# Kernel optimization log

Measured on AMD Instinct MI355X. Metric: run time of the kernel, lower is better.

Reference implementation:

```python
import jax, jax.numpy as jnp
import numpy as np

M_PARAM = 8          # M from __init__
NUM_INTERESTS = 32   # K, num_extracted_interests (max)


def setup_inputs() -> dict:
    key = jax.random.key(0)
    ks = jax.random.split(key, 6)
    bs, L, N, d, ic, K = 512, 100, 64, 256, 256, NUM_INTERESTS
    history = jax.random.normal(ks[0], (bs, L, d), dtype=jnp.float32)
    history_mask = jnp.ones((bs, L), dtype=bool)  # unused by the original forward, kept for signature fidelity
    candidates = jax.random.normal(ks[1], (bs, N, d), dtype=jnp.float32)
    num_extracted_interests = jnp.maximum(
        jax.random.randint(ks[2], (bs,), 0, K, dtype=jnp.int32), 1)
    unique_category_counts = jax.random.randint(ks[3], (bs,), 1, 19, dtype=jnp.int32)
    W = jax.random.normal(ks[4], (ic, d), dtype=jnp.float32) / np.sqrt(d)   # Linear(news_dim->interest_dim), no bias
    context_codes = jax.random.normal(ks[5], (K, ic), dtype=jnp.float32) / np.sqrt(ic)
    return {
        "history_news_representations": history,
        "history_mask": history_mask,
        "candidate_news_representations": candidates,
        "num_extracted_interests": num_extracted_interests,
        "unique_category_counts": unique_category_counts,
        "W": W,
        "context_codes": context_codes,
    }


def _user_encoder(history, candidates, num_interests, cat_counts, W, context_codes):
    bs, L, d = history.shape
    K = context_codes.shape[0]
    # ---- PolyAttention ----
    proj = jnp.tanh(jnp.einsum('bld,cd->blc', history, W))           # [bs, L, ic]
    scores = jnp.einsum('blc,kc->bkl', proj, context_codes)          # [bs, K, L]
    code_mask = jnp.arange(K)[None, :] < num_interests[:, None]      # [bs, K]
    scores = jnp.where(code_mask[:, :, None], scores, jnp.float32(-1e9))
    attn = jax.nn.softmax(scores, axis=2)                            # over history length L
    attn = jnp.nan_to_num(attn, nan=0.0, posinf=0.0, neginf=0.0)
    interests = jnp.einsum('bkl,bld->bkd', attn, history)            # [bs, K, d]
    # ---- InterestCandidateAttention, vectorized over all N candidates ----
    w = jnp.einsum('bkd,bnd->bnk', interests, candidates)            # [bs, N, K]
    dynK = jnp.clip(
        jnp.ceil(jnp.log2(M_PARAM * cat_counts.astype(jnp.float32))).astype(jnp.int32),
        1, K)                                                        # [bs]
    # variable-K top-k mask via descending ranks (values a.s. distinct)
    order = jnp.argsort(-w, axis=-1)
    ranks = jnp.argsort(order, axis=-1)                              # rank 0 = largest
    topk_mask = (ranks < dynK[:, None, None]).astype(w.dtype)        # [bs, N, K]
    masked = w * topk_mask
    user = jnp.einsum('bnk,bkd->bnd', masked, interests)             # [bs, N, d]
    return user


def reference(history_news_representations, history_mask, candidate_news_representations,
              num_extracted_interests, unique_category_counts, W, context_codes):
    return _user_encoder(history_news_representations, candidate_news_representations,
                         num_extracted_interests, unique_category_counts, W, context_codes)
```

## Files before the change

kernel.cpp:

```cpp
#include <hip/hip_runtime.h>
#include <hip/hip_bf16.h>

typedef __bf16 bf16_t;
typedef __bf16 bf16x8 __attribute__((ext_vector_type(8)));
typedef float  f32x4  __attribute__((ext_vector_type(4)));

#define BS 512
#define LH 100
#define NC 64
#define DD 256
#define IC 256
#define KK 32

#define OFF_WPL 6553600
#define OFF_CPL (6553600 + 3 * 131072)

__device__ __forceinline__ void split3(float v, bf16_t& h, bf16_t& l, bf16_t& l2) {
    h = (bf16_t)v;  float r1 = v - (float)h;
    l = (bf16_t)r1; float r2 = r1 - (float)l;
    l2 = (bf16_t)r2;
}

__device__ __forceinline__ void split3x8(const float* v, bf16x8& h, bf16x8& l, bf16x8& l2) {
#pragma unroll
    for (int j = 0; j < 8; j++) {
        bf16_t a, b, c;
        split3(v[j], a, b, c);
        h[j] = a; l[j] = b; l2[j] = c;
    }
}

__device__ __forceinline__ void mfma6(const bf16x8& ah, const bf16x8& al, const bf16x8& al2,
                                      const bf16x8& bh, const bf16x8& bl, const bf16x8& bl2,
                                      f32x4& accM, f32x4& accC) {
    accM = __builtin_amdgcn_mfma_f32_16x16x32_bf16(ah,  bh,  accM, 0, 0, 0);
    accC = __builtin_amdgcn_mfma_f32_16x16x32_bf16(ah,  bl,  accC, 0, 0, 0);
    accC = __builtin_amdgcn_mfma_f32_16x16x32_bf16(al,  bh,  accC, 0, 0, 0);
    accC = __builtin_amdgcn_mfma_f32_16x16x32_bf16(ah,  bl2, accC, 0, 0, 0);
    accC = __builtin_amdgcn_mfma_f32_16x16x32_bf16(al,  bl,  accC, 0, 0, 0);
    accC = __builtin_amdgcn_mfma_f32_16x16x32_bf16(al2, bh,  accC, 0, 0, 0);
}

__device__ __forceinline__ void mfma6s(const bf16x8& ah, const bf16x8& al, const bf16x8& al2,
                                       const bf16x8& bh, const bf16x8& bl, const bf16x8& bl2,
                                       f32x4& accM, f32x4& accC0, f32x4& accC1) {
    accM  = __builtin_amdgcn_mfma_f32_16x16x32_bf16(ah,  bh,  accM,  0, 0, 0);
    accC0 = __builtin_amdgcn_mfma_f32_16x16x32_bf16(ah,  bl,  accC0, 0, 0, 0);
    accC1 = __builtin_amdgcn_mfma_f32_16x16x32_bf16(al,  bh,  accC1, 0, 0, 0);
    accC0 = __builtin_amdgcn_mfma_f32_16x16x32_bf16(ah,  bl2, accC0, 0, 0, 0);
    accC1 = __builtin_amdgcn_mfma_f32_16x16x32_bf16(al,  bl,  accC1, 0, 0, 0);
    accC0 = __builtin_amdgcn_mfma_f32_16x16x32_bf16(al2, bh,  accC0, 0, 0, 0);
}

__device__ __forceinline__ float fast_tanh_f32(float xf) {
    const double t  = fabs((double)xf) * 2.0;
    const double nf = rint(t * 1.4426950408889634);
    double r = fma(nf, -6.93147180369123816490e-01, t);
    r = fma(nf, -1.90821492927058770002e-10, r);
    const double r2 = r * r;
    double p =        2.08767569878680989792e-09;
    p = fma(p, r,     2.50521083854417187751e-08);
    p = fma(p, r,     2.75573192239858906526e-07);
    p = fma(p, r,     2.75573192239858925110e-06);
    p = fma(p, r,     2.48015873015873015873e-05);
    p = fma(p, r,     1.98412698412698412526e-04);
    p = fma(p, r,     1.38888888888888894069e-03);
    p = fma(p, r,     8.33333333333333321769e-03);
    p = fma(p, r,     4.16666666666666643537e-02);
    p = fma(p, r,     1.66666666666666657415e-01);
    p = fma(p, r,     5.00000000000000000000e-01);
    const double q   = fma(r2, p, r);
    const double s   = ldexp(1.0, (int)nf);
    const double em1 = fma(s, q, s - 1.0);
    double ti = em1 / (em1 + 2.0);
    if (t > 20.0) ti = 1.0;
    return copysignf((float)ti, xf);
}

__device__ __forceinline__ double fast_exp_f64(double x) {
    const double nf = rint(x * 1.4426950408889634);
    double r = fma(nf, -6.93147180369123816490e-01, x);
    r = fma(nf, -1.90821492927058770002e-10, r);
    const double r2 = r * r;
    double p =        2.08767569878680989792e-09;
    p = fma(p, r,     2.50521083854417187751e-08);
    p = fma(p, r,     2.75573192239858906526e-07);
    p = fma(p, r,     2.75573192239858925110e-06);
    p = fma(p, r,     2.48015873015873015873e-05);
    p = fma(p, r,     1.98412698412698412526e-04);
    p = fma(p, r,     1.38888888888888894069e-03);
    p = fma(p, r,     8.33333333333333321769e-03);
    p = fma(p, r,     4.16666666666666643537e-02);
    p = fma(p, r,     1.66666666666666657415e-01);
    p = fma(p, r,     5.00000000000000000000e-01);
    const double q = fma(r2, p, r);
    const double s = ldexp(1.0, (int)nf);
    return fma(s, q, s);
}

__global__ __launch_bounds__(256) void kp_split(const float* __restrict__ W,
                                                const float* __restrict__ C,
                                                bf16_t* __restrict__ Wh, bf16_t* __restrict__ Wl,
                                                bf16_t* __restrict__ Wl2,
                                                bf16_t* __restrict__ Ch, bf16_t* __restrict__ Cl,
                                                bf16_t* __restrict__ Cl2) {
    int idx = blockIdx.x * 256 + threadIdx.x;
    if (idx < 65536) {
        bf16_t h, l, l2;
        split3(W[idx], h, l, l2);
        Wh[idx] = h; Wl[idx] = l; Wl2[idx] = l2;
    } else {
        int i = idx - 65536;
        if (i < 8192) {
            bf16_t h, l, l2;
            split3(C[i], h, l, l2);
            Ch[i] = h; Cl[i] = l; Cl2[i] = l2;
        }
    }
}

#define WCH 24576
__global__ __launch_bounds__(448) void k12_proj_scores(const float* __restrict__ H,
                                                       const bf16_t* __restrict__ Wh,
                                                       const bf16_t* __restrict__ Wl,
                                                       const bf16_t* __restrict__ Wl2,
                                                       const bf16_t* __restrict__ Ch,
                                                       const bf16_t* __restrict__ Cl,
                                                       const bf16_t* __restrict__ Cl2,
                                                       float* __restrict__ S) {
    __shared__ __align__(16) char wbuf[2][WCH];
    __shared__ float pl[7][16 * 34];

    const int tid = threadIdx.x;
    const int wave = tid >> 6;
    const int lane = tid & 63;
    const int r = lane & 15, q = lane >> 4;
    const int b = blockIdx.x;
    const int lrow0 = wave * 16;

    const bf16_t* it_base[4];
    int it_src[4], it_dst[4];
#pragma unroll
    for (int it = 0; it < 4; it++) {
        const int g = tid + it * 448;
        const int p = (g >> 9) & 3, rem = g & 511, row = rem >> 5, grp = rem & 31;
        it_base[it] = (p == 0) ? Wh : (p == 1) ? Wl : Wl2;
        it_src[it] = row * DD + grp * 8;
        it_dst[it] = (p * 16 + row) * 512 + ((grp * 16) ^ ((row & 7) << 4));
    }
    const bool has4 = (tid < 192);

    bf16x8 Ah[8], Al[8], Al2[8];
    {
        long grow = (long)b * LH + lrow0 + r;
        const long maxrow = (long)BS * LH - 1;
        if (grow > maxrow) grow = maxrow;
        const float* arow = H + (size_t)grow * DD + q * 8;
#pragma unroll
        for (int ks = 0; ks < 8; ks++) {
            const float* ap = arow + ks * 32;
            float4 u = *(const float4*)ap;
            float4 v = *(const float4*)(ap + 4);
            float av[8] = {u.x, u.y, u.z, u.w, v.x, v.y, v.z, v.w};
            split3x8(av, Ah[ks], Al[ks], Al2[ks]);
        }
    }

    const f32x4 zero = {0.f, 0.f, 0.f, 0.f};
    f32x4 saccM[2], saccC[2];
    saccM[0] = zero; saccM[1] = zero; saccC[0] = zero; saccC[1] = zero;

    float* myp = pl[wave];
    const int swz = (r & 7) << 4;

    {
        bf16x8 p0 = *(const bf16x8*)(it_base[0] + it_src[0]);
        bf16x8 p1 = *(const bf16x8*)(it_base[1] + it_src[1]);
        bf16x8 p2 = *(const bf16x8*)(it_base[2] + it_src[2]);
        bf16x8 p3;
        if (has4) p3 = *(const bf16x8*)(it_base[3] + it_src[3]);
        *(bf16x8*)(wbuf[0] + it_dst[0]) = p0;
        *(bf16x8*)(wbuf[0] + it_dst[1]) = p1;
        *(bf16x8*)(wbuf[0] + it_dst[2]) = p2;
        if (has4) *(bf16x8*)(wbuf[0] + it_dst[3]) = p3;
    }
    __syncthreads();

    for (int c16 = 0; c16 < 16; c16++) {
        const char* cur = wbuf[c16 & 1];
        char* nxt = wbuf[(c16 & 1) ^ 1];
        const bool pfv = (c16 < 15);

        bf16x8 p0, p1, p2, p3;
        if (pfv) {
            const int co = (c16 + 1) * 16 * DD;
            p0 = *(const bf16x8*)(it_base[0] + co + it_src[0]);
            p1 = *(const bf16x8*)(it_base[1] + co + it_src[1]);
            p2 = *(const bf16x8*)(it_base[2] + co + it_src[2]);
            if (has4) p3 = *(const bf16x8*)(it_base[3] + co + it_src[3]);
        }

        f32x4 aM = zero, aC0 = zero, aC1 = zero;
#pragma unroll
        for (int ks = 0; ks < 8; ks++) {
            const int colb = (ks * 64 + q * 16) ^ swz;
            const char* rowp = cur + r * 512 + colb;
            bf16x8 bh  = *(const bf16x8*)(rowp);
            bf16x8 bl  = *(const bf16x8*)(rowp + 8192);
            bf16x8 bl2 = *(const bf16x8*)(rowp + 16384);
            mfma6s(Ah[ks], Al[ks], Al2[ks], bh, bl, bl2, aM, aC0, aC1);
        }

        const int colb2 = (c16 & 1) * 16;
#pragma unroll
        for (int i = 0; i < 4; i++) {
            float s1 = aM[i] + aC0[i] + aC1[i];
            myp[(q * 4 + i) * 34 + colb2 + r] = fast_tanh_f32(s1);
        }

        if (c16 & 1) {
            const int c0 = (c16 >> 1) * 32;
            const float* ps = myp + r * 34 + q * 8;
            float pv[8];
#pragma unroll
            for (int j = 0; j < 8; j++) pv[j] = ps[j];
            bf16x8 ph, plo, pl2;
            split3x8(pv, ph, plo, pl2);
#pragma unroll
            for (int ntS = 0; ntS < 2; ntS++) {
                const size_t base = (size_t)(ntS * 16 + r) * IC + c0 + q * 8;
                bf16x8 ch  = *(const bf16x8*)(Ch  + base);
                bf16x8 cl  = *(const bf16x8*)(Cl  + base);
                bf16x8 cl2 = *(const bf16x8*)(Cl2 + base);
                mfma6(ph, plo, pl2, ch, cl, cl2, saccM[ntS], saccC[ntS]);
            }
        }

        if (pfv) {
            *(bf16x8*)(nxt + it_dst[0]) = p0;
            *(bf16x8*)(nxt + it_dst[1]) = p1;
            *(bf16x8*)(nxt + it_dst[2]) = p2;
            if (has4) *(bf16x8*)(nxt + it_dst[3]) = p3;
        }
        __syncthreads();
    }

#pragma unroll
    for (int ntS = 0; ntS < 2; ntS++)
#pragma unroll
        for (int i = 0; i < 4; i++) {
            const int lrow = lrow0 + q * 4 + i;
            if (lrow < LH)
                S[((size_t)b * LH + lrow) * KK + ntS * 16 + r] = saccM[ntS][i] + saccC[ntS][i];
        }
}

__global__ __launch_bounds__(512) void k3456_fused(const float* __restrict__ Sg,
                                                   const int* __restrict__ ni,
                                                   const int* __restrict__ cc,
                                                   const float* __restrict__ H,
                                                   const float* __restrict__ cand,
                                                   float* __restrict__ out) {
    __shared__ __align__(16) char smem[47616];
    float*  attn_l = (float*)smem;
    float*  ls     = (float*)(smem + 12800);
    double* red    = (double*)(smem + 25600);
    float*  ht     = (float*)(smem + 12800);
    float*  I_l    = (float*)(smem + 12800);
    float*  shw    = (float*)smem;

    const int b = blockIdx.x;
    const int tid = threadIdx.x;
    const int wave = tid >> 6;
    const int lane = tid & 63;
    const int r = lane & 15, q = lane >> 4;
    const f32x4 zero = {0.f, 0.f, 0.f, 0.f};

    {
        const float* Sb = Sg + (size_t)b * LH * KK;
        for (int i = tid; i < LH * KK; i += 512) ls[i] = Sb[i];
        __syncthreads();

        const int k = tid & 31;
        const int grp = tid >> 5;
        const bool act = (grp < 8);
        const int nib = ni[b];

        double vals[13];
        if (act) {
            double vmax = -1e300;
#pragma unroll
            for (int i = 0; i < 13; i++) {
                const int l = grp + 8 * i;
                double v = (l < LH) ? (double)ls[l * KK + k] : -1e300;
                vals[i] = v;
                vmax = fmax(vmax, v);
            }
            red[grp * 33 + k] = vmax;
        }
        __syncthreads();
        if (tid < 32) {
            double m = red[k];
            for (int j = 1; j < 8; j++) m = fmax(m, red[j * 33 + k]);
            red[k] = m;
        }
        __syncthreads();
        const double mx = red[k];
        __syncthreads();

        if (act) {
            double s = 0.0;
#pragma unroll
            for (int i = 0; i < 13; i++) {
                const int l = grp + 8 * i;
                if (l < LH) {
                    double e = fast_exp_f64(vals[i] - mx);
                    vals[i] = e;
                    s += e;
                }
            }
            red[grp * 33 + k] = s;
        }
        __syncthreads();
        if (tid < 32) {
            double t = 0.0;
            for (int j = 0; j < 8; j++) t += red[j * 33 + k];
            red[k] = t;
        }
        __syncthreads();
        const double inv = 1.0 / red[k];

        if (act) {
            float* ab = attn_l + k * LH;
            const bool masked = (k >= nib);
#pragma unroll
            for (int i = 0; i < 13; i++) {
                const int l = grp + 8 * i;
                if (l < LH) ab[l] = masked ? 0.01f : (float)(vals[i] * inv);
            }
        }
    }
    __syncthreads();

    {
        const float* Hb = H + (size_t)b * LH * DD;
        const int mtB = wave & 1;
        const int m0B = mtB * 16;

        f32x4 accM[4], accC[4];
#pragma unroll
        for (int jj = 0; jj < 4; jj++) { accM[jj] = zero; accC[jj] = zero; }

        for (int ks = 0; ks < 4; ks++) {
            const int l0c = ks * 32;
            __syncthreads();
            for (int u = tid; u < 32 * 64; u += 512) {
                const int l = u >> 6, dg = u & 63;
                float4 v = {0.f, 0.f, 0.f, 0.f};
                if (l0c + l < LH) v = *(const float4*)(Hb + (size_t)(l0c + l) * DD + dg * 4);
                ht[(dg * 4 + 0) * 34 + l] = v.x;
                ht[(dg * 4 + 1) * 34 + l] = v.y;
                ht[(dg * 4 + 2) * 34 + l] = v.z;
                ht[(dg * 4 + 3) * 34 + l] = v.w;
            }
            __syncthreads();

            float av[8];
#pragma unroll
            for (int j = 0; j < 8; j++) {
                const int l = l0c + q * 8 + j;
                av[j] = (l < LH) ? attn_l[(m0B + r) * LH + l] : 0.f;
            }
            bf16x8 ah, al, al2;
            split3x8(av, ah, al, al2);

#pragma unroll
            for (int jj = 0; jj < 4; jj++) {
                const int job = wave + jj * 8;
                const int nt = job >> 1;
                const int n0 = nt * 16;
                float bv[8];
                const float* hp = ht + (n0 + r) * 34 + q * 8;
#pragma unroll
                for (int j = 0; j < 8; j++) bv[j] = hp[j];
                bf16x8 bh, bl, bl2;
                split3x8(bv, bh, bl, bl2);
                mfma6(ah, al, al2, bh, bl, bl2, accM[jj], accC[jj]);
            }
        }
        __syncthreads();

#pragma unroll
        for (int jj = 0; jj < 4; jj++) {
            const int job = wave + jj * 8;
            const int nt = job >> 1;
            const int n0 = nt * 16;
#pragma unroll
            for (int i = 0; i < 4; i++)
                I_l[(m0B + q * 4 + i) * 260 + n0 + r] = accM[jj][i] + accC[jj][i];
        }
    }
    __syncthreads();

    {
        const float* Cb = cand + (size_t)b * NC * DD;
        const int job = wave;
        const int mt = job >> 1, nt = job & 1;
        const int m0 = mt * 16, n0 = nt * 16;
        f32x4 accM = zero, accC = zero;
#pragma unroll
        for (int ks = 0; ks < 8; ks++) {
            const float* ap = Cb + (size_t)(m0 + r) * DD + ks * 32 + q * 8;
            const float* bp = I_l + (n0 + r) * 260 + ks * 32 + q * 8;
            float4 u1 = *(const float4*)ap;      float4 u2 = *(const float4*)(ap + 4);
            float4 v1 = *(const float4*)bp;      float4 v2 = *(const float4*)(bp + 4);
            float av[8] = {u1.x,u1.y,u1.z,u1.w,u2.x,u2.y,u2.z,u2.w};
            float bv[8] = {v1.x,v1.y,v1.z,v1.w,v2.x,v2.y,v2.z,v2.w};
            bf16x8 ah, al, al2, bh, bl, bl2;
            split3x8(av, ah, al, al2);
            split3x8(bv, bh, bl, bl2);
            mfma6(ah, al, al2, bh, bl, bl2, accM, accC);
        }
#pragma unroll
        for (int i = 0; i < 4; i++) shw[(m0 + q * 4 + i) * 33 + n0 + r] = accM[i] + accC[i];

        __syncthreads();

        {
            const int n = tid & 63;
            const int kg = tid >> 6;
            int c8 = 8 * cc[b];
            int dynK = 32 - __clz(c8 - 1);
            dynK = min(max(dynK, 1), KK);
            float v[KK];
#pragma unroll
            for (int j = 0; j < KK; j++) v[j] = shw[n * 33 + j];
            float keep[4];
#pragma unroll
            for (int j = 0; j < 4; j++) {
                const int kk2 = kg + 8 * j;
                int rank = 0;
#pragma unroll
                for (int jj = 0; jj < KK; jj++)
                    rank += (v[jj] > v[kk2]) || (v[jj] == v[kk2] && jj < kk2);
                keep[j] = (rank < dynK) ? v[kk2] : 0.f;
            }
            __syncthreads();
#pragma unroll
            for (int j = 0; j < 4; j++)
                shw[n * 33 + kg + 8 * j] = keep[j];
        }
    }
    __syncthreads();

    {
        const int d = tid & 255;
        const int nh = tid >> 8;
        float icol[KK];
#pragma unroll
        for (int k = 0; k < KK; k++) icol[k] = I_l[k * 260 + d];

        const int nend = nh * 32 + 32;
        for (int n = nh * 32; n < nend; n++) {
            const float* wr = shw + n * 33;
            float acc = 0.f;
#pragma unroll
            for (int k = 0; k < KK; k++) acc += wr[k] * icol[k];
            out[((size_t)b * NC + n) * DD + d] = acc;
        }
    }
}

extern "C" void kernel_launch(void* const* d_in, const int* in_sizes, int n_in,
                              void* d_out, int out_size, void* d_ws, size_t ws_size,
                              hipStream_t stream) {
    const float* hist = (const float*)d_in[0];
    const float* cand = (const float*)d_in[2];
    const int* ni = (const int*)d_in[3];
    const int* cc = (const int*)d_in[4];
    const float* W = (const float*)d_in[5];
    const float* C = (const float*)d_in[6];
    float* out = (float*)d_out;

    char* w8 = (char*)d_ws;
    float*  S   = (float*)(w8 + 0);
    bf16_t* Wh  = (bf16_t*)(w8 + OFF_WPL);
    bf16_t* Wl  = (bf16_t*)(w8 + OFF_WPL + 131072);
    bf16_t* Wl2 = (bf16_t*)(w8 + OFF_WPL + 262144);
    bf16_t* Ch  = (bf16_t*)(w8 + OFF_CPL);
    bf16_t* Cl  = (bf16_t*)(w8 + OFF_CPL + 16384);
    bf16_t* Cl2 = (bf16_t*)(w8 + OFF_CPL + 32768);

    kp_split<<<288, 256, 0, stream>>>(W, C, Wh, Wl, Wl2, Ch, Cl, Cl2);
    k12_proj_scores<<<BS, 448, 0, stream>>>(hist, Wh, Wl, Wl2, Ch, Cl, Cl2, S);
    k3456_fused<<<BS, 512, 0, stream>>>(S, ni, cc, hist, cand, out);
}
```

Measured before the change: 232.0 us.

## Use a dedicated producer wave for W tile staging in proj-scores kernel

```diff
diff --git a/kernel.cpp b/kernel.cpp
--- a/kernel.cpp
+++ b/kernel.cpp
@@ -120,7 +120,7 @@
 }
 
 #define WCH 24576
-__global__ __launch_bounds__(448) void k12_proj_scores(const float* __restrict__ H,
+__global__ __launch_bounds__(512) void k12_proj_scores(const float* __restrict__ H,
                                                        const bf16_t* __restrict__ Wh,
                                                        const bf16_t* __restrict__ Wl,
                                                        const bf16_t* __restrict__ Wl2,
@@ -136,22 +136,25 @@
     const int lane = tid & 63;
     const int r = lane & 15, q = lane >> 4;
     const int b = blockIdx.x;
+    const bool producer = (wave == 7);
     const int lrow0 = wave * 16;
 
-    const bf16_t* it_base[4];
-    int it_src[4], it_dst[4];
-#pragma unroll
-    for (int it = 0; it < 4; it++) {
-        const int g = tid + it * 448;
-        const int p = (g >> 9) & 3, rem = g & 511, row = rem >> 5, grp = rem & 31;
-        it_base[it] = (p == 0) ? Wh : (p == 1) ? Wl : Wl2;
-        it_src[it] = row * DD + grp * 8;
-        it_dst[it] = (p * 16 + row) * 512 + ((grp * 16) ^ ((row & 7) << 4));
-    }
-    const bool has4 = (tid < 192);
+    const f32x4 zero = {0.f, 0.f, 0.f, 0.f};
+    f32x4 saccM[2], saccC[2];
+    saccM[0] = zero; saccM[1] = zero; saccC[0] = zero; saccC[1] = zero;
 
     bf16x8 Ah[8], Al[8], Al2[8];
-    {
+
+    if (producer) {
+#pragma unroll 4
+        for (int it = 0; it < 24; it++) {
+            const int g = lane + it * 64;
+            const int p = g >> 9, rem = g & 511, row = rem >> 5, grp = rem & 31;
+            const bf16_t* src = (p == 0) ? Wh : (p == 1) ? Wl : Wl2;
+            bf16x8 v = *(const bf16x8*)(src + row * DD + grp * 8);
+            *(bf16x8*)(wbuf[0] + (p * 16 + row) * 512 + ((grp * 16) ^ ((row & 7) << 4))) = v;
+        }
+    } else {
         long grow = (long)b * LH + lrow0 + r;
         const long maxrow = (long)BS * LH - 1;
         if (grow > maxrow) grow = maxrow;
@@ -165,94 +168,77 @@
             split3x8(av, Ah[ks], Al[ks], Al2[ks]);
         }
     }
-
-    const f32x4 zero = {0.f, 0.f, 0.f, 0.f};
-    f32x4 saccM[2], saccC[2];
-    saccM[0] = zero; saccM[1] = zero; saccC[0] = zero; saccC[1] = zero;
-
-    float* myp = pl[wave];
+    __syncthreads();
+
+    float* myp = pl[wave & 7];
     const int swz = (r & 7) << 4;
-
-    {
-        bf16x8 p0 = *(const bf16x8*)(it_base[0] + it_src[0]);
-        bf16x8 p1 = *(const bf16x8*)(it_base[1] + it_src[1]);
-        bf16x8 p2 = *(const bf16x8*)(it_base[2] + it_src[2]);
-        bf16x8 p3;
-        if (has4) p3 = *(const bf16x8*)(it_base[3] + it_src[3]);
-        *(bf16x8*)(wbuf[0] + it_dst[0]) = p0;
-        *(bf16x8*)(wbuf[0] + it_dst[1]) = p1;
-        *(bf16x8*)(wbuf[0] + it_dst[2]) = p2;
-        if (has4) *(bf16x8*)(wbuf[0] + it_dst[3]) = p3;
-    }
-    __syncthreads();
 
     for (int c16 = 0; c16 < 16; c16++) {
         const char* cur = wbuf[c16 & 1];
         char* nxt = wbuf[(c16 & 1) ^ 1];
-        const bool pfv = (c16 < 15);
-
-        bf16x8 p0, p1, p2, p3;
-        if (pfv) {
-            const int co = (c16 + 1) * 16 * DD;
-            p0 = *(const bf16x8*)(it_base[0] + co + it_src[0]);
-            p1 = *(const bf16x8*)(it_base[1] + co + it_src[1]);
-            p2 = *(const bf16x8*)(it_base[2] + co + it_src[2]);
-            if (has4) p3 = *(const bf16x8*)(it_base[3] + co + it_src[3]);
-        }
-
-        f32x4 aM = zero, aC0 = zero, aC1 = zero;
-#pragma unroll
-        for (int ks = 0; ks < 8; ks++) {
-            const int colb = (ks * 64 + q * 16) ^ swz;
-            const char* rowp = cur + r * 512 + colb;
-            bf16x8 bh  = *(const bf16x8*)(rowp);
-            bf16x8 bl  = *(const bf16x8*)(rowp + 8192);
-            bf16x8 bl2 = *(const bf16x8*)(rowp + 16384);
-            mfma6s(Ah[ks], Al[ks], Al2[ks], bh, bl, bl2, aM, aC0, aC1);
-        }
-
-        const int colb2 = (c16 & 1) * 16;
-#pragma unroll
-        for (int i = 0; i < 4; i++) {
-            float s1 = aM[i] + aC0[i] + aC1[i];
-            myp[(q * 4 + i) * 34 + colb2 + r] = fast_tanh_f32(s1);
-        }
-
-        if (c16 & 1) {
-            const int c0 = (c16 >> 1) * 32;
-            const float* ps = myp + r * 34 + q * 8;
-            float pv[8];
-#pragma unroll
-            for (int j = 0; j < 8; j++) pv[j] = ps[j];
-            bf16x8 ph, plo, pl2;
-            split3x8(pv, ph, plo, pl2);
-#pragma unroll
-            for (int ntS = 0; ntS < 2; ntS++) {
-                const size_t base = (size_t)(ntS * 16 + r) * IC + c0 + q * 8;
-                bf16x8 ch  = *(const bf16x8*)(Ch  + base);
-                bf16x8 cl  = *(const bf16x8*)(Cl  + base);
-                bf16x8 cl2 = *(const bf16x8*)(Cl2 + base);
-                mfma6(ph, plo, pl2, ch, cl, cl2, saccM[ntS], saccC[ntS]);
-            }
-        }
-
-        if (pfv) {
-            *(bf16x8*)(nxt + it_dst[0]) = p0;
-            *(bf16x8*)(nxt + it_dst[1]) = p1;
-            *(bf16x8*)(nxt + it_dst[2]) = p2;
-            if (has4) *(bf16x8*)(nxt + it_dst[3]) = p3;
-        }
-        __syncthreads();
-    }
-
-#pragma unroll
-    for (int ntS = 0; ntS < 2; ntS++)
-#pragma unroll
-        for (int i = 0; i < 4; i++) {
-            const int lrow = lrow0 + q * 4 + i;
-            if (lrow < LH)
-                S[((size_t)b * LH + lrow) * KK + ntS * 16 + r] = saccM[ntS][i] + saccC[ntS][i];
-        }
+
+        if (producer) {
+            if (c16 < 15) {
+                const int co = (c16 + 1) * 16 * DD;
+#pragma unroll 4
+                for (int it = 0; it < 24; it++) {
+                    const int g = lane + it * 64;
+                    const int p = g >> 9, rem = g & 511, row = rem >> 5, grp = rem & 31;
+                    const bf16_t* src = (p == 0) ? Wh : (p == 1) ? Wl : Wl2;
+                    bf16x8 v = *(const bf16x8*)(src + co + row * DD + grp * 8);
+                    *(bf16x8*)(nxt + (p * 16 + row) * 512 + ((grp * 16) ^ ((row & 7) << 4))) = v;
+                }
+            }
+        } else {
+            f32x4 aM = zero, aC0 = zero, aC1 = zero;
+#pragma unroll
+            for (int ks = 0; ks < 8; ks++) {
+                const int colb = (ks * 64 + q * 16) ^ swz;
+                const char* rowp = cur + r * 512 + colb;
+                bf16x8 bh  = *(const bf16x8*)(rowp);
+                bf16x8 bl  = *(const bf16x8*)(rowp + 8192);
+                bf16x8 bl2 = *(const bf16x8*)(rowp + 16384);
+                mfma6s(Ah[ks], Al[ks], Al2[ks], bh, bl, bl2, aM, aC0, aC1);
+            }
+
+            const int colb2 = (c16 & 1) * 16;
+#pragma unroll
+            for (int i = 0; i < 4; i++) {
+                float s1 = aM[i] + aC0[i] + aC1[i];
+                myp[(q * 4 + i) * 34 + colb2 + r] = fast_tanh_f32(s1);
+            }
+
+            if (c16 & 1) {
+                const int c0 = (c16 >> 1) * 32;
+                const float* ps = myp + r * 34 + q * 8;
+                float pv[8];
+#pragma unroll
+                for (int j = 0; j < 8; j++) pv[j] = ps[j];
+                bf16x8 ph, plo, pl2;
+                split3x8(pv, ph, plo, pl2);
+#pragma unroll
+                for (int ntS = 0; ntS < 2; ntS++) {
+                    const size_t base = (size_t)(ntS * 16 + r) * IC + c0 + q * 8;
+                    bf16x8 ch  = *(const bf16x8*)(Ch  + base);
+                    bf16x8 cl  = *(const bf16x8*)(Cl  + base);
+                    bf16x8 cl2 = *(const bf16x8*)(Cl2 + base);
+                    mfma6(ph, plo, pl2, ch, cl, cl2, saccM[ntS], saccC[ntS]);
+                }
+            }
+        }
+        __syncthreads();
+    }
+
+    if (!producer) {
+#pragma unroll
+        for (int ntS = 0; ntS < 2; ntS++)
+#pragma unroll
+            for (int i = 0; i < 4; i++) {
+                const int lrow = lrow0 + q * 4 + i;
+                if (lrow < LH)
+                    S[((size_t)b * LH + lrow) * KK + ntS * 16 + r] = saccM[ntS][i] + saccC[ntS][i];
+            }
+    }
 }
 
 __global__ __launch_bounds__(512) void k3456_fused(const float* __restrict__ Sg,
@@ -492,6 +478,6 @@
     bf16_t* Cl2 = (bf16_t*)(w8 + OFF_CPL + 32768);
 
     kp_split<<<288, 256, 0, stream>>>(W, C, Wh, Wl, Wl2, Ch, Cl, Cl2);
-    k12_proj_scores<<<BS, 448, 0, stream>>>(hist, Wh, Wl, Wl2, Ch, Cl, Cl2, S);
+    k12_proj_scores<<<BS, 512, 0, stream>>>(hist, Wh, Wl, Wl2, Ch, Cl, Cl2, S);
     k3456_fused<<<BS, 512, 0, stream>>>(S, ni, cc, hist, cand, out);
 }
```

Result: slower. 249.4 us (+7.5%).

## Process 32-column W chunks per iteration with single-buffered LDS staging

Applied to the files above, without the earlier changes.

```diff
diff --git a/kernel.cpp b/kernel.cpp
--- a/kernel.cpp
+++ b/kernel.cpp
@@ -119,7 +119,6 @@
     }
 }
 
-#define WCH 24576
 __global__ __launch_bounds__(448) void k12_proj_scores(const float* __restrict__ H,
                                                        const bf16_t* __restrict__ Wh,
                                                        const bf16_t* __restrict__ Wl,
@@ -128,7 +127,7 @@
                                                        const bf16_t* __restrict__ Cl,
                                                        const bf16_t* __restrict__ Cl2,
                                                        float* __restrict__ S) {
-    __shared__ __align__(16) char wbuf[2][WCH];
+    __shared__ __align__(16) char wbuf[49152];
     __shared__ float pl[7][16 * 34];
 
     const int tid = threadIdx.x;
@@ -138,17 +137,19 @@
     const int b = blockIdx.x;
     const int lrow0 = wave * 16;
 
-    const bf16_t* it_base[4];
-    int it_src[4], it_dst[4];
-#pragma unroll
-    for (int it = 0; it < 4; it++) {
+    const bf16_t* it_base[7];
+    int it_src[7], it_dst[7];
+#pragma unroll
+    for (int it = 0; it < 7; it++) {
         const int g = tid + it * 448;
-        const int p = (g >> 9) & 3, rem = g & 511, row = rem >> 5, grp = rem & 31;
+        const int p0 = g >> 10;
+        const int p = (p0 > 2) ? 2 : p0;
+        const int rem = g & 1023, row = rem >> 5, grp = rem & 31;
         it_base[it] = (p == 0) ? Wh : (p == 1) ? Wl : Wl2;
         it_src[it] = row * DD + grp * 8;
-        it_dst[it] = (p * 16 + row) * 512 + ((grp * 16) ^ ((row & 7) << 4));
-    }
-    const bool has4 = (tid < 192);
+        it_dst[it] = (p * 32 + row) * 512 + ((grp * 16) ^ ((row & 7) << 4));
+    }
+    const bool has7 = (tid < 384);
 
     bf16x8 Ah[8], Al[8], Al2[8];
     {
@@ -174,52 +175,55 @@
     const int swz = (r & 7) << 4;
 
     {
-        bf16x8 p0 = *(const bf16x8*)(it_base[0] + it_src[0]);
-        bf16x8 p1 = *(const bf16x8*)(it_base[1] + it_src[1]);
-        bf16x8 p2 = *(const bf16x8*)(it_base[2] + it_src[2]);
-        bf16x8 p3;
-        if (has4) p3 = *(const bf16x8*)(it_base[3] + it_src[3]);
-        *(bf16x8*)(wbuf[0] + it_dst[0]) = p0;
-        *(bf16x8*)(wbuf[0] + it_dst[1]) = p1;
-        *(bf16x8*)(wbuf[0] + it_dst[2]) = p2;
-        if (has4) *(bf16x8*)(wbuf[0] + it_dst[3]) = p3;
+#pragma unroll
+        for (int it = 0; it < 7; it++)
+            if (it < 6 || has7) {
+                bf16x8 v = *(const bf16x8*)(it_base[it] + it_src[it]);
+                *(bf16x8*)(wbuf + it_dst[it]) = v;
+            }
     }
     __syncthreads();
 
-    for (int c16 = 0; c16 < 16; c16++) {
-        const char* cur = wbuf[c16 & 1];
-        char* nxt = wbuf[(c16 & 1) ^ 1];
-        const bool pfv = (c16 < 15);
-
-        bf16x8 p0, p1, p2, p3;
-        if (pfv) {
-            const int co = (c16 + 1) * 16 * DD;
-            p0 = *(const bf16x8*)(it_base[0] + co + it_src[0]);
-            p1 = *(const bf16x8*)(it_base[1] + co + it_src[1]);
-            p2 = *(const bf16x8*)(it_base[2] + co + it_src[2]);
-            if (has4) p3 = *(const bf16x8*)(it_base[3] + co + it_src[3]);
-        }
-
-        f32x4 aM = zero, aC0 = zero, aC1 = zero;
+    for (int pr = 0; pr < 8; pr++) {
+        bf16x8 pf[7];
+        if (pr < 7) {
+            const int co = (pr + 1) * 8192;
+#pragma unroll
+            for (int it = 0; it < 7; it++)
+                if (it < 6 || has7)
+                    pf[it] = *(const bf16x8*)(it_base[it] + co + it_src[it]);
+        }
+
+        f32x4 aM0 = zero, aC00 = zero, aC01 = zero;
+        f32x4 aM1 = zero, aC10 = zero, aC11 = zero;
 #pragma unroll
         for (int ks = 0; ks < 8; ks++) {
             const int colb = (ks * 64 + q * 16) ^ swz;
-            const char* rowp = cur + r * 512 + colb;
-            bf16x8 bh  = *(const bf16x8*)(rowp);
-            bf16x8 bl  = *(const bf16x8*)(rowp + 8192);
-            bf16x8 bl2 = *(const bf16x8*)(rowp + 16384);
-            mfma6s(Ah[ks], Al[ks], Al2[ks], bh, bl, bl2, aM, aC0, aC1);
-        }
-
-        const int colb2 = (c16 & 1) * 16;
+            const char* b0 = wbuf + r * 512 + colb;
+            const char* b1 = wbuf + (16 + r) * 512 + colb;
+            bf16x8 bh0  = *(const bf16x8*)(b0);
+            bf16x8 bl0  = *(const bf16x8*)(b0 + 16384);
+            bf16x8 bl20 = *(const bf16x8*)(b0 + 32768);
+            bf16x8 bh1  = *(const bf16x8*)(b1);
+            bf16x8 bl1  = *(const bf16x8*)(b1 + 16384);
+            bf16x8 bl21 = *(const bf16x8*)(b1 + 32768);
+            mfma6s(Ah[ks], Al[ks], Al2[ks], bh0, bl0, bl20, aM0, aC00, aC01);
+            mfma6s(Ah[ks], Al[ks], Al2[ks], bh1, bl1, bl21, aM1, aC10, aC11);
+        }
+
 #pragma unroll
         for (int i = 0; i < 4; i++) {
-            float s1 = aM[i] + aC0[i] + aC1[i];
-            myp[(q * 4 + i) * 34 + colb2 + r] = fast_tanh_f32(s1);
-        }
-
-        if (c16 & 1) {
-            const int c0 = (c16 >> 1) * 32;
+            float s0 = aM0[i] + aC00[i] + aC01[i];
+            myp[(q * 4 + i) * 34 + r] = fast_tanh_f32(s0);
+        }
+#pragma unroll
+        for (int i = 0; i < 4; i++) {
+            float s1 = aM1[i] + aC10[i] + aC11[i];
+            myp[(q * 4 + i) * 34 + 16 + r] = fast_tanh_f32(s1);
+        }
+
+        {
+            const int c0 = pr * 32;
             const float* ps = myp + r * 34 + q * 8;
             float pv[8];
 #pragma unroll
@@ -236,11 +240,12 @@
             }
         }
 
-        if (pfv) {
-            *(bf16x8*)(nxt + it_dst[0]) = p0;
-            *(bf16x8*)(nxt + it_dst[1]) = p1;
-            *(bf16x8*)(nxt + it_dst[2]) = p2;
-            if (has4) *(bf16x8*)(nxt + it_dst[3]) = p3;
+        __syncthreads();
+        if (pr < 7) {
+#pragma unroll
+            for (int it = 0; it < 7; it++)
+                if (it < 6 || has7)
+                    *(bf16x8*)(wbuf + it_dst[it]) = pf[it];
         }
         __syncthreads();
     }
```

After: 287.0 us. +23.7%, slower.
